# Optimization experiments

Hardware: AMD Instinct MI355X
Metric: run time of the kernel (lower is better)

The kernel has to match this reference:

```python
import jax, jax.numpy as jnp
import numpy as np

N_NODES = 100000
NEG_SLOPE = 0.2
EPS = 1e-16


def gat_conv(x, src, dst, W, a_src, a_dst, bias, heads, out_dim, concat):
    # x: [N, F]; src/dst: [Etot] (self loops already appended)
    N = x.shape[0]
    h = (x @ W).reshape(N, heads, out_dim)          # [N, H, D]
    alpha_src = jnp.einsum('nhd,hd->nh', h, a_src)  # [N, H]
    alpha_dst = jnp.einsum('nhd,hd->nh', h, a_dst)  # [N, H]
    e = alpha_src[src] + alpha_dst[dst]             # [E, H]
    e = jnp.where(e > 0, e, NEG_SLOPE * e)          # leaky_relu
    # segment softmax over incoming edges of each dst node
    m = jax.ops.segment_max(e, dst, num_segments=N)
    e = jnp.exp(e - m[dst])
    s = jax.ops.segment_sum(e, dst, num_segments=N)
    alpha = e / (s[dst] + EPS)                      # [E, H]
    msg = h[src] * alpha[:, :, None]                # [E, H, D]
    out = jax.ops.segment_sum(msg, dst, num_segments=N)  # [N, H, D]
    if concat:
        out = out.reshape(N, heads * out_dim)
    else:
        out = out.mean(axis=1)
    return out + bias


def setup_inputs() -> dict:
    key = jax.random.key(0)
    ks = jax.random.split(key, 10)
    F_in, H1, D1 = 256, 8, 8
    D2 = 256 // 2  # hidden_features // 2
    x = jax.random.normal(ks[0], (N_NODES, F_in), dtype=jnp.float32)
    edge_index = jax.random.randint(ks[1], (2, 1600000), 0, N_NODES, dtype=jnp.int64)
    sc1 = 1.0 / np.sqrt(F_in)
    sc2 = 1.0 / np.sqrt(H1 * D1)
    return {
        'x': x,
        'edge_index': edge_index,
        'W1': jax.random.normal(ks[2], (F_in, H1 * D1), dtype=jnp.float32) * sc1,
        'a_src1': jax.random.normal(ks[3], (H1, D1), dtype=jnp.float32) * 0.1,
        'a_dst1': jax.random.normal(ks[4], (H1, D1), dtype=jnp.float32) * 0.1,
        'b1': jnp.zeros((H1 * D1,), dtype=jnp.float32),
        'W2': jax.random.normal(ks[5], (H1 * D1, D2), dtype=jnp.float32) * sc2,
        'a_src2': jax.random.normal(ks[6], (1, D2), dtype=jnp.float32) * 0.1,
        'a_dst2': jax.random.normal(ks[7], (1, D2), dtype=jnp.float32) * 0.1,
        'b2': jnp.zeros((D2,), dtype=jnp.float32),
    }


def reference(x, edge_index, W1, a_src1, a_dst1, b1, W2, a_src2, a_dst2, b2):
    # GAT.encode in eval mode (dropout p=0.6 disabled)
    N = x.shape[0]
    loop = jnp.arange(N, dtype=edge_index.dtype)
    src = jnp.concatenate([edge_index[0], loop])  # PyG add_self_loops
    dst = jnp.concatenate([edge_index[1], loop])
    h = gat_conv(x, src, dst, W1, a_src1, a_dst1, b1, heads=8, out_dim=8, concat=True)
    h = jax.nn.elu(h)
    z = gat_conv(h, src, dst, W2, a_src2, a_dst2, b2, heads=1, out_dim=128, concat=False)
    return z
```

## Files before the change

kernel.cpp:

```cpp
#include <hip/hip_runtime.h>
#include <hip/hip_bf16.h>
#include <cstdint>

#define H1 8
#define C1 64
#define D2 128
#define FIN 256
#define NEG 0.2f
#define EPSS 1e-16f
#define CH 1024
#define XPAD 264
#define XQ 72
#define HP 68
#define NPBIN 128
#define TILEB 4096
#define MAXD1 128
#define MAXD2 256

template<typename T> __device__ __forceinline__ float toF(T v);
template<> __device__ __forceinline__ float toF<float>(float v) { return v; }
template<> __device__ __forceinline__ float toF<__hip_bfloat16>(__hip_bfloat16 v) { return __bfloat162float(v); }
template<typename T> __device__ __forceinline__ T fromF(float v);
template<> __device__ __forceinline__ float fromF<float>(float v) { return v; }
template<> __device__ __forceinline__ __hip_bfloat16 fromF<__hip_bfloat16>(float v) { return __float2bfloat16(v); }

__device__ __forceinline__ float bcast_lane(float v, int lane) {
    return __int_as_float(__builtin_amdgcn_readlane(__float_as_int(v), lane));
}

__device__ __forceinline__ unsigned pk_bf16(float lo, float hi) {
    unsigned a = (unsigned)__bfloat16_as_ushort(__float2bfloat16(lo));
    unsigned b = (unsigned)__bfloat16_as_ushort(__float2bfloat16(hi));
    return a | (b << 16);
}

__device__ __forceinline__ float bf16u_toF(unsigned short u) {
    unsigned v = ((unsigned)u) << 16;
    return __uint_as_float(v);
}

typedef __attribute__((ext_vector_type(8))) short bf16x8;
typedef __attribute__((ext_vector_type(4))) float f32x4;

__device__ __forceinline__ void chain_upd(float ev, float hv,
                                          float& m, float& s, float& a)
{
    float mn = fmaxf(m, ev);
    float sc = __expf(m - mn);
    float p  = __expf(ev - mn);
    s = fmaf(s, sc, p);
    a = fmaf(a, sc, p * hv);
    m = mn;
}

__global__ __launch_bounds__(256) void k_wcvt(const float* __restrict__ W1,
    unsigned short* __restrict__ Wb)
{
    int t = blockIdx.x * 256 + threadIdx.x;
    int c = t >> 7, kp = t & 127;
    if (c < C1) {
        float f0 = W1[(2 * kp) * C1 + c];
        float f1 = W1[(2 * kp + 1) * C1 + c];
        *reinterpret_cast<unsigned*>(&Wb[c * XPAD + 2 * kp]) = pk_bf16(f0, f1);
    }
}

__global__ __launch_bounds__(256) void k_w2cvt(const float* __restrict__ W2,
    unsigned short* __restrict__ W2b)
{
    int t = blockIdx.x * 256 + threadIdx.x;
    if (t < C1 * D2 / 2) {
        float f0 = W2[2 * t], f1 = W2[2 * t + 1];
        *reinterpret_cast<unsigned*>(&W2b[2 * t]) = pk_bf16(f0, f1);
    }
}

template<typename T>
__global__ __launch_bounds__(256) void k_gemm1(const float* __restrict__ x,
    const unsigned short* __restrict__ Wb, const float* __restrict__ a_src1,
    const float* __restrict__ a_dst1, T* __restrict__ h1,
    float* __restrict__ asrc1, float* __restrict__ adst1, int N)
{
    __shared__ alignas(16) char smem[2 * 64 * XQ * 2];
    unsigned short* Xs = (unsigned short*)smem;
    unsigned short* Wt = (unsigned short*)(smem + 64 * XQ * 2);
    int tid = threadIdx.x;
    int wave = tid >> 6, lane = tid & 63;
    int nodeBase = blockIdx.x * 64;
    int m = lane & 15, kg = lane >> 4;
    int arow = wave * 16 + m;

    f32x4 acc[4];
    #pragma unroll
    for (int t = 0; t < 4; ++t) acc[t] = (f32x4){0.f, 0.f, 0.f, 0.f};

    #pragma unroll
    for (int kh = 0; kh < 4; ++kh) {
        for (int i = tid; i < 512; i += 256) {
            int c = i >> 3, ch = i & 7;
            *reinterpret_cast<uint4*>(&Wt[c * XQ + ch * 8]) =
                *reinterpret_cast<const uint4*>(&Wb[c * XPAD + kh * 64 + ch * 8]);
        }
        for (int i = tid; i < 1024; i += 256) {
            int r = i >> 4, q = i & 15;
            int n = nodeBase + r;
            float4 v = (n < N) ? reinterpret_cast<const float4*>(x)[(size_t)n * 64 + kh * 16 + q]
                               : make_float4(0.f, 0.f, 0.f, 0.f);
            *reinterpret_cast<uint2*>(&Xs[r * XQ + q * 4]) =
                make_uint2(pk_bf16(v.x, v.y), pk_bf16(v.z, v.w));
        }
        __syncthreads();
        #pragma unroll
        for (int ks = 0; ks < 2; ++ks) {
            int k0 = ks * 32 + kg * 8;
            bf16x8 a = *reinterpret_cast<const bf16x8*>(&Xs[arow * XQ + k0]);
            #pragma unroll
            for (int t = 0; t < 4; ++t) {
                bf16x8 b = *reinterpret_cast<const bf16x8*>(&Wt[(t * 16 + m) * XQ + k0]);
                acc[t] = __builtin_amdgcn_mfma_f32_16x16x32_bf16(a, b, acc[t], 0, 0, 0);
            }
        }
        __syncthreads();
    }

    float* Hs = reinterpret_cast<float*>(smem);
    int crow = (lane >> 4) * 4;
    #pragma unroll
    for (int t = 0; t < 4; ++t)
        #pragma unroll
        for (int r = 0; r < 4; ++r)
            Hs[(wave * 16 + crow + r) * HP + t * 16 + m] = acc[t][r];
    __syncthreads();

    float as_l = a_src1[lane], ad_l = a_dst1[lane];
    int n0 = nodeBase + wave * 16;
    #pragma unroll
    for (int i = 0; i < 16; ++i) {
        int n = n0 + i;
        if (n >= N) break;
        float hv = Hs[(wave * 16 + i) * HP + lane];
        h1[(size_t)n * C1 + lane] = fromF<T>(hv);
        float vs = hv * as_l, vd = hv * ad_l;
        #pragma unroll
        for (int off = 1; off < 8; off <<= 1) {
            vs += __shfl_xor(vs, off);
            vd += __shfl_xor(vd, off);
        }
        if ((lane & 7) == 0) {
            asrc1[n * H1 + (lane >> 3)] = vs;
            adst1[n * H1 + (lane >> 3)] = vd;
        }
    }
}

__global__ __launch_bounds__(128) void k_wvec(const float* __restrict__ W2,
    const float* __restrict__ a_src2, const float* __restrict__ a_dst2,
    float* __restrict__ wsrc, float* __restrict__ wdst)
{
    int t = threadIdx.x;
    int k = t & 63;
    const float* a = (t < 64) ? a_src2 : a_dst2;
    float s = 0.f;
    for (int c = 0; c < D2; ++c) s = fmaf(W2[k * D2 + c], a[c], s);
    if (t < 64) wsrc[k] = s; else wdst[k] = s;
}

__global__ __launch_bounds__(256) void k_binhist(const int* __restrict__ ei, int E, int N,
    int nbins, int* __restrict__ binCnt)
{
    __shared__ int lcnt[1024];
    int tot = E + N;
    int t0 = blockIdx.x * TILEB;
    int cnt = min(TILEB, tot - t0);
    for (int i = threadIdx.x; i < nbins; i += 256) lcnt[i] = 0;
    __syncthreads();
    for (int i = threadIdx.x; i < cnt; i += 256) {
        int e = t0 + i;
        int dst = (e < E) ? ei[(size_t)E + e] : (e - E);
        atomicAdd(&lcnt[dst >> 7], 1);
    }
    __syncthreads();
    for (int i = threadIdx.x; i < nbins; i += 256)
        if (lcnt[i]) atomicAdd(&binCnt[i], lcnt[i]);
}

__global__ __launch_bounds__(256) void k_binscan(const int* __restrict__ binCnt,
    int* __restrict__ binOff, int* __restrict__ binCur, int nbins)
{
    __shared__ int wtot[4];
    int t = threadIdx.x, lane = t & 63, wave = t >> 6;
    int v[4];
    #pragma unroll
    for (int j = 0; j < 4; ++j) {
        int idx = t * 4 + j;
        v[j] = (idx < nbins) ? binCnt[idx] : 0;
    }
    int s = v[0] + v[1] + v[2] + v[3];
    int incl = s;
    #pragma unroll
    for (int off = 1; off < 64; off <<= 1) {
        int tt = __shfl_up(incl, off);
        if (lane >= off) incl += tt;
    }
    if (lane == 63) wtot[wave] = incl;
    __syncthreads();
    int woff = 0;
    #pragma unroll
    for (int w = 0; w < 4; ++w) if (w < wave) woff += wtot[w];
    int run = woff + incl - s;
    #pragma unroll
    for (int j = 0; j < 4; ++j) {
        int idx = t * 4 + j;
        if (idx < nbins) { binOff[idx] = run; binCur[idx] = run; }
        run += v[j];
    }
    if (t == 255) binOff[nbins] = woff + incl;
}

__global__ __launch_bounds__(256) void k_bin(const int* __restrict__ ei, int E, int N,
    int nbins, int* __restrict__ binCur, int* __restrict__ binned)
{
    __shared__ int recs[TILEB];
    __shared__ unsigned short bns[TILEB];
    __shared__ int lcnt[1024];
    __shared__ int lbase[1024];
    int tot = E + N;
    int t0 = blockIdx.x * TILEB;
    int cnt = min(TILEB, tot - t0);
    for (int i = threadIdx.x; i < nbins; i += 256) lcnt[i] = 0;
    __syncthreads();
    for (int i = threadIdx.x; i < cnt; i += 256) {
        int e = t0 + i;
        int src, dst;
        if (e < E) { src = ei[e]; dst = ei[(size_t)E + e]; }
        else       { src = e - E; dst = src; }
        int b = dst >> 7;
        recs[i] = src | ((dst & 127) << 17);
        bns[i] = (unsigned short)b;
        atomicAdd(&lcnt[b], 1);
    }
    __syncthreads();
    for (int i = threadIdx.x; i < nbins; i += 256) {
        int c = lcnt[i];
        if (c) lbase[i] = atomicAdd(&binCur[i], c);
        lcnt[i] = 0;
    }
    __syncthreads();
    for (int i = threadIdx.x; i < cnt; i += 256) {
        int b = bns[i];
        int lp = atomicAdd(&lcnt[b], 1);
        binned[lbase[b] + lp] = recs[i];
    }
}

__global__ __launch_bounds__(256) void k_binptr(const int* __restrict__ binOff,
    const int* __restrict__ binned, int* __restrict__ ptr,
    int* __restrict__ edge_src, int N, int nbins)
{
    __shared__ int cnt[NPBIN];
    __shared__ int cur[NPBIN];
    __shared__ int w0tot;
    int b = blockIdx.x, t = threadIdx.x;
    int s0 = binOff[b], s1 = binOff[b + 1];
    if (t < NPBIN) cnt[t] = 0;
    __syncthreads();
    for (int i = s0 + t; i < s1; i += 256)
        atomicAdd(&cnt[binned[i] >> 17], 1);
    __syncthreads();
    int v = 0, incl = 0;
    if (t < NPBIN) {
        int lane = t & 63;
        v = cnt[t];
        incl = v;
        #pragma unroll
        for (int off = 1; off < 64; off <<= 1) {
            int tt = __shfl_up(incl, off);
            if (lane >= off) incl += tt;
        }
        if (t == 63) w0tot = incl;
    }
    __syncthreads();
    if (t < NPBIN) {
        int base = s0 + ((t >= 64) ? w0tot : 0);
        int excl = base + incl - v;
        int node = b * NPBIN + t;
        if (node < N) ptr[node] = excl;
        cur[t] = excl;
    }
    if (b == nbins - 1 && t == 0) ptr[N] = s1;
    __syncthreads();
    for (int i = s0 + t; i < s1; i += 256) {
        int rec = binned[i];
        int p = atomicAdd(&cur[rec >> 17], 1);
        edge_src[p] = rec & 0x1FFFF;
    }
}

__global__ void k_count(const int* __restrict__ ei, int E, int N,
                        int* __restrict__ deg)
{
    int tot = E + N;
    for (int e = blockIdx.x * blockDim.x + threadIdx.x; e < tot;
         e += gridDim.x * blockDim.x) {
        int dst = (e < E) ? ei[(size_t)E + e] : (e - E);
        atomicAdd(&deg[dst], 1);
    }
}

__global__ void k_scatter(const int* __restrict__ ei, int E, int N,
                          int* __restrict__ cursor, int* __restrict__ edge_src)
{
    int tot = E + N;
    for (int e = blockIdx.x * blockDim.x + threadIdx.x; e < tot;
         e += gridDim.x * blockDim.x) {
        int src, dst;
        if (e < E) { src = ei[e]; dst = ei[(size_t)E + e]; }
        else       { src = e - E; dst = e - E; }
        int pos = atomicAdd(&cursor[dst], 1);
        edge_src[pos] = src;
    }
}

__global__ __launch_bounds__(256) void k_scanA(const int* __restrict__ deg,
    int* __restrict__ ptr, int* __restrict__ chunkSum)
{
    __shared__ int wtot[4];
    int b = blockIdx.x, t = threadIdx.x;
    int lane = t & 63, wave = t >> 6;
    int4 v = reinterpret_cast<const int4*>(deg + (size_t)b * CH)[t];
    int s = v.x + v.y + v.z + v.w;
    int incl = s;
    #pragma unroll
    for (int off = 1; off < 64; off <<= 1) {
        int tt = __shfl_up(incl, off);
        if (lane >= off) incl += tt;
    }
    if (lane == 63) wtot[wave] = incl;
    __syncthreads();
    int woff = 0;
    #pragma unroll
    for (int w = 0; w < 4; ++w) if (w < wave) woff += wtot[w];
    int excl = woff + incl - s;
    int i0 = b * CH + t * 4;
    ptr[i0 + 0] = excl;
    ptr[i0 + 1] = excl + v.x;
    ptr[i0 + 2] = excl + v.x + v.y;
    ptr[i0 + 3] = excl + v.x + v.y + v.z;
    if (t == 255) chunkSum[b] = woff + incl;
}

__global__ void k_scanB(const int* __restrict__ chunkSum, int* __restrict__ chunkOff,
                        int NB, int* __restrict__ ptrN)
{
    if (threadIdx.x == 0) {
        int c = 0;
        for (int b = 0; b < NB; ++b) { chunkOff[b] = c; c += chunkSum[b]; }
        *ptrN = c;
    }
}

__global__ __launch_bounds__(256) void k_scanC(int* __restrict__ ptr,
    int* __restrict__ cursor, const int* __restrict__ chunkOff, int N)
{
    int b = blockIdx.x;
    int off = chunkOff[b];
    int i0 = b * CH + threadIdx.x * 4;
    #pragma unroll
    for (int k = 0; k < 4; ++k) {
        int i = i0 + k;
        if (i < N) { int v = ptr[i] + off; ptr[i] = v; cursor[i] = v; }
    }
}

template<typename T>
__global__ __launch_bounds__(256) void k_agg1(const int* __restrict__ ptr,
    const int* __restrict__ edge_src, const T* __restrict__ h1,
    const float* __restrict__ asrc1, const float* __restrict__ adst1,
    const float* __restrict__ b1, const float* __restrict__ wsrc,
    const float* __restrict__ wdst, T* __restrict__ hmid,
    float* __restrict__ asrc2, float* __restrict__ adst2, int N)
{
    __shared__ float S1[4 * MAXD1 * H1];
    int wave = threadIdx.x >> 6, lane = threadIdx.x & 63;
    float* st = S1 + wave * (MAXD1 * H1);
    int n = blockIdx.x * 4 + wave;
    if (n >= N) return;
    int start = ptr[n], end = ptr[n + 1];
    int deg = end - start;
    int h = lane >> 3;
    float o;

    if (deg <= MAXD1) {
        int e_loc = lane >> 3, hh = lane & 7;
        float adsth = adst1[n * H1 + hh];
        float mloc = -1e30f;
        for (int eb = start, base = 0; eb < end; eb += 8, base += 64) {
            int e = eb + e_loc;
            float ev = -1e30f;
            if (e < end) {
                int s = edge_src[e];
                ev = asrc1[s * H1 + hh] + adsth;
                ev = ev > 0.f ? ev : NEG * ev;
                st[base + lane] = ev;
            }
            mloc = fmaxf(mloc, ev);
        }
        mloc = fmaxf(mloc, __shfl_xor(mloc, 8));
        mloc = fmaxf(mloc, __shfl_xor(mloc, 16));
        mloc = fmaxf(mloc, __shfl_xor(mloc, 32));
        __builtin_amdgcn_wave_barrier();
        float sloc = 0.f;
        for (int eb = start, base = 0; eb < end; eb += 8, base += 64) {
            if (eb + e_loc < end) {
                float p = __expf(st[base + lane] - mloc);
                st[base + lane] = p;
                sloc += p;
            }
        }
        sloc += __shfl_xor(sloc, 8);
        sloc += __shfl_xor(sloc, 16);
        sloc += __shfl_xor(sloc, 32);
        float inv = 1.f / (sloc + EPSS);
        __builtin_amdgcn_wave_barrier();
        float inv_c = __shfl(inv, h);

        float a0 = 0.f, a1 = 0.f, a2 = 0.f, a3 = 0.f;
        float a4 = 0.f, a5 = 0.f, a6 = 0.f, a7 = 0.f;
        int e = start;
        for (; e + 8 <= end; e += 8) {
            int r = e - start;
            int i0 = edge_src[e + 0]; int i1 = edge_src[e + 1];
            int i2 = edge_src[e + 2]; int i3 = edge_src[e + 3];
            int i4 = edge_src[e + 4]; int i5 = edge_src[e + 5];
            int i6 = edge_src[e + 6]; int i7 = edge_src[e + 7];
            float w0 = st[(r + 0) * H1 + h]; float w1 = st[(r + 1) * H1 + h];
            float w2 = st[(r + 2) * H1 + h]; float w3 = st[(r + 3) * H1 + h];
            float w4 = st[(r + 4) * H1 + h]; float w5 = st[(r + 5) * H1 + h];
            float w6 = st[(r + 6) * H1 + h]; float w7 = st[(r + 7) * H1 + h];
            a0 = fmaf(w0, toF(h1[((size_t)(unsigned)i0 << 6) + lane]), a0);
            a1 = fmaf(w1, toF(h1[((size_t)(unsigned)i1 << 6) + lane]), a1);
            a2 = fmaf(w2, toF(h1[((size_t)(unsigned)i2 << 6) + lane]), a2);
            a3 = fmaf(w3, toF(h1[((size_t)(unsigned)i3 << 6) + lane]), a3);
            a4 = fmaf(w4, toF(h1[((size_t)(unsigned)i4 << 6) + lane]), a4);
            a5 = fmaf(w5, toF(h1[((size_t)(unsigned)i5 << 6) + lane]), a5);
            a6 = fmaf(w6, toF(h1[((size_t)(unsigned)i6 << 6) + lane]), a6);
            a7 = fmaf(w7, toF(h1[((size_t)(unsigned)i7 << 6) + lane]), a7);
        }
        for (; e < end; ++e) {
            int s = edge_src[e];
            a0 = fmaf(st[(e - start) * H1 + h],
                      toF(h1[((size_t)(unsigned)s << 6) + lane]), a0);
        }
        float acc = ((a0 + a1) + (a2 + a3)) + ((a4 + a5) + (a6 + a7));
        o = acc * inv_c;
    } else {
        float adst = adst1[n * H1 + h];
        float m[8], ss[8], aa[8];
        #pragma unroll
        for (int j = 0; j < 8; ++j) { m[j] = -1e30f; ss[j] = 0.f; aa[j] = 0.f; }
        int e = start;
        for (; e + 8 <= end; e += 8) {
            int idx[8];
            #pragma unroll
            for (int j = 0; j < 8; ++j) idx[j] = edge_src[e + j];
            #pragma unroll
            for (int j = 0; j < 8; ++j) {
                float t = asrc1[idx[j] * H1 + h] + adst;
                t = t > 0.f ? t : NEG * t;
                chain_upd(t, toF(h1[((size_t)(unsigned)idx[j] << 6) + lane]),
                          m[j], ss[j], aa[j]);
            }
        }
        for (; e < end; ++e) {
            int s = edge_src[e];
            float t = asrc1[s * H1 + h] + adst;
            t = t > 0.f ? t : NEG * t;
            chain_upd(t, toF(h1[((size_t)(unsigned)s << 6) + lane]), m[0], ss[0], aa[0]);
        }
        float M = fmaxf(fmaxf(fmaxf(m[0], m[1]), fmaxf(m[2], m[3])),
                        fmaxf(fmaxf(m[4], m[5]), fmaxf(m[6], m[7])));
        float sum = 0.f, acc = 0.f;
        #pragma unroll
        for (int j = 0; j < 8; ++j) {
            float sc = __expf(m[j] - M);
            sum = fmaf(ss[j], sc, sum);
            acc = fmaf(aa[j], sc, acc);
        }
        o = acc / (sum + EPSS);
    }

    o = o + b1[lane];
    o = o > 0.f ? o : (expf(o) - 1.f);
    hmid[(size_t)n * C1 + lane] = fromF<T>(o);
    float vs = o * wsrc[lane];
    float vd = o * wdst[lane];
    #pragma unroll
    for (int off = 1; off < 64; off <<= 1) {
        vs += __shfl_xor(vs, off);
        vd += __shfl_xor(vd, off);
    }
    if (lane == 0) { asrc2[n] = vs; adst2[n] = vd; }
}

template<typename T>
__global__ __launch_bounds__(256) void k_agg2out(const int* __restrict__ ptr,
    const int* __restrict__ edge_src, const T* __restrict__ hmid,
    const float* __restrict__ asrc2, const float* __restrict__ adst2,
    const unsigned short* __restrict__ W2b, const float* __restrict__ b2,
    float* __restrict__ out, int N)
{
    __shared__ unsigned short Ws[C1 * D2];
    __shared__ float S2[4 * MAXD2];
    for (int i = threadIdx.x; i < C1 * D2 / 8; i += 256)
        reinterpret_cast<uint4*>(Ws)[i] = reinterpret_cast<const uint4*>(W2b)[i];
    __syncthreads();

    int wave = threadIdx.x >> 6, lane = threadIdx.x & 63;
    float* st = S2 + wave * MAXD2;
    int n = blockIdx.x * 4 + wave;
    if (n >= N) return;
    int start = ptr[n], end = ptr[n + 1];
    int deg = end - start;
    float adst = adst2[n];
    float aggv;

    if (deg <= MAXD2) {
        float mloc = -1e30f;
        for (int e = start + lane; e < end; e += 64) {
            int s = edge_src[e];
            float ev = asrc2[s] + adst;
            ev = ev > 0.f ? ev : NEG * ev;
            st[e - start] = ev;
            mloc = fmaxf(mloc, ev);
        }
        #pragma unroll
        for (int off = 1; off < 64; off <<= 1)
            mloc = fmaxf(mloc, __shfl_xor(mloc, off));
        __builtin_amdgcn_wave_barrier();
        float sloc = 0.f;
        for (int e = start + lane; e < end; e += 64) {
            float p = __expf(st[e - start] - mloc);
            st[e - start] = p;
            sloc += p;
        }
        #pragma unroll
        for (int off = 1; off < 64; off <<= 1)
            sloc += __shfl_xor(sloc, off);
        float inv = 1.f / (sloc + EPSS);
        __builtin_amdgcn_wave_barrier();

        float a0 = 0.f, a1 = 0.f, a2 = 0.f, a3 = 0.f;
        float a4 = 0.f, a5 = 0.f, a6 = 0.f, a7 = 0.f;
        int e = start;
        for (; e + 8 <= end; e += 8) {
            int r = e - start;
            int i0 = edge_src[e + 0]; int i1 = edge_src[e + 1];
            int i2 = edge_src[e + 2]; int i3 = edge_src[e + 3];
            int i4 = edge_src[e + 4]; int i5 = edge_src[e + 5];
            int i6 = edge_src[e + 6]; int i7 = edge_src[e + 7];
            a0 = fmaf(st[r + 0], toF(hmid[((size_t)(unsigned)i0 << 6) + lane]), a0);
            a1 = fmaf(st[r + 1], toF(hmid[((size_t)(unsigned)i1 << 6) + lane]), a1);
            a2 = fmaf(st[r + 2], toF(hmid[((size_t)(unsigned)i2 << 6) + lane]), a2);
            a3 = fmaf(st[r + 3], toF(hmid[((size_t)(unsigned)i3 << 6) + lane]), a3);
            a4 = fmaf(st[r + 4], toF(hmid[((size_t)(unsigned)i4 << 6) + lane]), a4);
            a5 = fmaf(st[r + 5], toF(hmid[((size_t)(unsigned)i5 << 6) + lane]), a5);
            a6 = fmaf(st[r + 6], toF(hmid[((size_t)(unsigned)i6 << 6) + lane]), a6);
            a7 = fmaf(st[r + 7], toF(hmid[((size_t)(unsigned)i7 << 6) + lane]), a7);
        }
        for (; e < end; ++e) {
            int s = edge_src[e];
            a0 = fmaf(st[e - start], toF(hmid[((size_t)(unsigned)s << 6) + lane]), a0);
        }
        float acc = ((a0 + a1) + (a2 + a3)) + ((a4 + a5) + (a6 + a7));
        aggv = acc * inv;
    } else {
        float m[8], ss[8], aa[8];
        #pragma unroll
        for (int j = 0; j < 8; ++j) { m[j] = -1e30f; ss[j] = 0.f; aa[j] = 0.f; }
        int e = start;
        for (; e + 8 <= end; e += 8) {
            int idx[8];
            #pragma unroll
            for (int j = 0; j < 8; ++j) idx[j] = edge_src[e + j];
            #pragma unroll
            for (int j = 0; j < 8; ++j) {
                float t = asrc2[idx[j]] + adst;
                t = t > 0.f ? t : NEG * t;
                chain_upd(t, toF(hmid[((size_t)(unsigned)idx[j] << 6) + lane]),
                          m[j], ss[j], aa[j]);
            }
        }
        for (; e < end; ++e) {
            int s = edge_src[e];
            float t = asrc2[s] + adst;
            t = t > 0.f ? t : NEG * t;
            chain_upd(t, toF(hmid[((size_t)(unsigned)s << 6) + lane]), m[0], ss[0], aa[0]);
        }
        float M = fmaxf(fmaxf(fmaxf(m[0], m[1]), fmaxf(m[2], m[3])),
                        fmaxf(fmaxf(m[4], m[5]), fmaxf(m[6], m[7])));
        float sum = 0.f, acc = 0.f;
        #pragma unroll
        for (int j = 0; j < 8; ++j) {
            float sc = __expf(m[j] - M);
            sum = fmaf(ss[j], sc, sum);
            acc = fmaf(aa[j], sc, acc);
        }
        aggv = acc / (sum + EPSS);
    }

    float acc0 = 0.f, acc1 = 0.f;
    #pragma unroll
    for (int k = 0; k < 64; ++k) {
        float xk = bcast_lane(aggv, k);
        float w0 = bf16u_toF(Ws[k * D2 + lane]);
        float w1 = bf16u_toF(Ws[k * D2 + 64 + lane]);
        acc0 = fmaf(xk, w0, acc0);
        acc1 = fmaf(xk, w1, acc1);
    }
    out[(size_t)n * D2 + lane]      = acc0 + b2[lane];
    out[(size_t)n * D2 + 64 + lane] = acc1 + b2[64 + lane];
}

extern "C" void kernel_launch(void* const* d_in, const int* in_sizes, int n_in,
                              void* d_out, int out_size, void* d_ws, size_t ws_size,
                              hipStream_t stream)
{
    const float* x      = (const float*)d_in[0];
    const int*   ei     = (const int*)d_in[1];
    const float* W1     = (const float*)d_in[2];
    const float* a_src1 = (const float*)d_in[3];
    const float* a_dst1 = (const float*)d_in[4];
    const float* b1     = (const float*)d_in[5];
    const float* W2     = (const float*)d_in[6];
    const float* a_src2 = (const float*)d_in[7];
    const float* a_dst2 = (const float*)d_in[8];
    const float* b2     = (const float*)d_in[9];
    float* out = (float*)d_out;

    const int N = in_sizes[0] / FIN;
    const int E = in_sizes[1] / 2;
    const int Etot = E + N;
    const int NB = (N + CH - 1) / CH;
    const size_t NP = (size_t)NB * CH;

    const size_t common =
        ((size_t)N * H1 * 4 + 255 & ~(size_t)255) * 2 +
        (((size_t)N * 4 + 255) & ~(size_t)255) * 2 +
        512 +
        (((size_t)NP * 4 + 255) & ~(size_t)255) * 2 +
        (((size_t)(NP + 1) * 4 + 255) & ~(size_t)255) +
        (((size_t)NB * 4 + 255) & ~(size_t)255) * 2 +
        (((size_t)Etot * 4 + 255) & ~(size_t)255) +
        (64 * XPAD * 2 + 256) +
        (C1 * D2 * 2 + 256) +
        4096;
    const bool f32path = ws_size >= common + 2 * ((size_t)N * C1 * 4 + 256);

    char* ws = (char*)d_ws;
    size_t off = 0;
    auto alloc = [&](size_t bytes) -> void* {
        void* p = ws + off;
        off = (off + bytes + 255) & ~(size_t)255;
        return p;
    };
    const size_t es = f32path ? 4 : 2;
    void*  h1v    = alloc((size_t)N * C1 * es);
    void*  hmidv  = alloc((size_t)N * C1 * es);
    float* asrc1  = (float*)alloc((size_t)N * H1 * 4);
    float* adst1  = (float*)alloc((size_t)N * H1 * 4);
    float* asrc2  = (float*)alloc((size_t)N * 4);
    float* adst2  = (float*)alloc((size_t)N * 4);
    float* wsrc   = (float*)alloc(64 * 4);
    float* wdst   = (float*)alloc(64 * 4);
    int*   deg    = (int*)alloc(NP * 4);
    int*   ptr    = (int*)alloc((NP + 1) * 4);
    int*   cursor = (int*)alloc(NP * 4);
    int*   chunkSum = (int*)alloc((size_t)NB * 4);
    int*   chunkOff = (int*)alloc((size_t)NB * 4);
    int*   edge_src = (int*)alloc((size_t)Etot * 4);
    unsigned short* Wb  = (unsigned short*)alloc(64 * XPAD * 2);
    unsigned short* W2b = (unsigned short*)alloc(C1 * D2 * 2);

    const int nodeBlocks = (N + 3) / 4;
    const int g1Blocks = (N + 63) / 64;

    k_wcvt<<<32, 256, 0, stream>>>(W1, Wb);
    k_w2cvt<<<16, 256, 0, stream>>>(W2, W2b);

    const int nbins = (N + NPBIN - 1) / NPBIN;
    const bool binpath = (N <= (1 << 17)) &&
                         ((size_t)Etot * 4 <= (size_t)N * C1 * es);
    if (binpath) {
        int* binned = (int*)h1v;
        int* binCnt = (int*)hmidv;
        int* binOff = binCnt + 1056;
        int* binCur = binOff + 1056;
        const int binBlocks = (Etot + TILEB - 1) / TILEB;
        hipMemsetAsync(binCnt, 0, (size_t)nbins * 4, stream);
        k_binhist<<<binBlocks, 256, 0, stream>>>(ei, E, N, nbins, binCnt);
        k_binscan<<<1, 256, 0, stream>>>(binCnt, binOff, binCur, nbins);
        k_bin<<<binBlocks, 256, 0, stream>>>(ei, E, N, nbins, binCur, binned);
        k_binptr<<<nbins, 256, 0, stream>>>(binOff, binned, ptr, edge_src, N, nbins);
    } else {
        hipMemsetAsync(deg, 0, NP * 4, stream);
        k_count<<<2048, 256, 0, stream>>>(ei, E, N, deg);
        k_scanA<<<NB, 256, 0, stream>>>(deg, ptr, chunkSum);
        k_scanB<<<1, 64, 0, stream>>>(chunkSum, chunkOff, NB, ptr + N);
        k_scanC<<<NB, 256, 0, stream>>>(ptr, cursor, chunkOff, N);
        k_scatter<<<2048, 256, 0, stream>>>(ei, E, N, cursor, edge_src);
    }

    k_wvec<<<1, 128, 0, stream>>>(W2, a_src2, a_dst2, wsrc, wdst);

    if (f32path) {
        float* h1 = (float*)h1v; float* hmid = (float*)hmidv;
        k_gemm1<float><<<g1Blocks, 256, 0, stream>>>(x, Wb, a_src1, a_dst1, h1, asrc1, adst1, N);
        k_agg1<float><<<nodeBlocks, 256, 0, stream>>>(ptr, edge_src, h1, asrc1, adst1, b1,
                                                      wsrc, wdst, hmid, asrc2, adst2, N);
        k_agg2out<float><<<nodeBlocks, 256, 0, stream>>>(ptr, edge_src, hmid, asrc2, adst2,
                                                         W2b, b2, out, N);
    } else {
        __hip_bfloat16* h1 = (__hip_bfloat16*)h1v; __hip_bfloat16* hmid = (__hip_bfloat16*)hmidv;
        k_gemm1<__hip_bfloat16><<<g1Blocks, 256, 0, stream>>>(x, Wb, a_src1, a_dst1, h1, asrc1, adst1, N);
        k_agg1<__hip_bfloat16><<<nodeBlocks, 256, 0, stream>>>(ptr, edge_src, h1, asrc1, adst1, b1,
                                                               wsrc, wdst, hmid, asrc2, adst2, N);
        k_agg2out<__hip_bfloat16><<<nodeBlocks, 256, 0, stream>>>(ptr, edge_src, hmid, asrc2, adst2,
                                                                  W2b, b2, out, N);
    }
}
```

Before: 335.6 us.

## Split layer-2 aggregation from output GEMM and merge weight prep kernels

Splits the fused aggregation-plus-projection kernel into two. The aggregation kernel writes the 64-wide aggregated vector to a scratch buffer, and a separate GEMM kernel computes 8 nodes per wave, so each shared-memory W2 load is reused across several nodes. The aggregation kernel no longer loads 16 KB of weights into LDS per block of 4 nodes. The three small weight-prep kernels become one launch. In exchange, the aggregated intermediate makes an extra round trip through global memory and one more kernel launch is added.

```diff
diff --git a/kernel.cpp b/kernel.cpp
--- a/kernel.cpp
+++ b/kernel.cpp
@@ -9,6 +9,8 @@
 #define NEG 0.2f
 #define EPSS 1e-16f
 #define CH 1024
+#define NPW2 8
+#define NPB2 32
 #define XPAD 264
 #define XQ 72
 #define HP 68
@@ -53,25 +55,36 @@
     m = mn;
 }
 
-__global__ __launch_bounds__(256) void k_wcvt(const float* __restrict__ W1,
-    unsigned short* __restrict__ Wb)
-{
-    int t = blockIdx.x * 256 + threadIdx.x;
-    int c = t >> 7, kp = t & 127;
-    if (c < C1) {
-        float f0 = W1[(2 * kp) * C1 + c];
-        float f1 = W1[(2 * kp + 1) * C1 + c];
-        *reinterpret_cast<unsigned*>(&Wb[c * XPAD + 2 * kp]) = pk_bf16(f0, f1);
-    }
-}
-
-__global__ __launch_bounds__(256) void k_w2cvt(const float* __restrict__ W2,
-    unsigned short* __restrict__ W2b)
-{
-    int t = blockIdx.x * 256 + threadIdx.x;
-    if (t < C1 * D2 / 2) {
-        float f0 = W2[2 * t], f1 = W2[2 * t + 1];
-        *reinterpret_cast<unsigned*>(&W2b[2 * t]) = pk_bf16(f0, f1);
+__global__ __launch_bounds__(256) void k_wprep(const float* __restrict__ W1,
+    const float* __restrict__ W2, const float* __restrict__ a_src2,
+    const float* __restrict__ a_dst2, unsigned short* __restrict__ Wb,
+    unsigned short* __restrict__ W2b, float* __restrict__ wsrc,
+    float* __restrict__ wdst)
+{
+    int b = blockIdx.x;
+    if (b < 32) {
+        int t = b * 256 + threadIdx.x;
+        int c = t >> 7, kp = t & 127;
+        if (c < C1) {
+            float f0 = W1[(2 * kp) * C1 + c];
+            float f1 = W1[(2 * kp + 1) * C1 + c];
+            *reinterpret_cast<unsigned*>(&Wb[c * XPAD + 2 * kp]) = pk_bf16(f0, f1);
+        }
+    } else if (b < 48) {
+        int t = (b - 32) * 256 + threadIdx.x;
+        if (t < C1 * D2 / 2) {
+            float f0 = W2[2 * t], f1 = W2[2 * t + 1];
+            *reinterpret_cast<unsigned*>(&W2b[2 * t]) = pk_bf16(f0, f1);
+        }
+    } else {
+        int t = threadIdx.x;
+        if (t < 128) {
+            int k = t & 63;
+            const float* a = (t < 64) ? a_src2 : a_dst2;
+            float s = 0.f;
+            for (int c = 0; c < D2; ++c) s = fmaf(W2[k * D2 + c], a[c], s);
+            if (t < 64) wsrc[k] = s; else wdst[k] = s;
+        }
     }
 }
 
@@ -151,18 +164,6 @@
             adst1[n * H1 + (lane >> 3)] = vd;
         }
     }
-}
-
-__global__ __launch_bounds__(128) void k_wvec(const float* __restrict__ W2,
-    const float* __restrict__ a_src2, const float* __restrict__ a_dst2,
-    float* __restrict__ wsrc, float* __restrict__ wdst)
-{
-    int t = threadIdx.x;
-    int k = t & 63;
-    const float* a = (t < 64) ? a_src2 : a_dst2;
-    float s = 0.f;
-    for (int c = 0; c < D2; ++c) s = fmaf(W2[k * D2 + c], a[c], s);
-    if (t < 64) wsrc[k] = s; else wdst[k] = s;
 }
 
 __global__ __launch_bounds__(256) void k_binhist(const int* __restrict__ ei, int E, int N,
@@ -503,18 +504,12 @@
 }
 
 template<typename T>
-__global__ __launch_bounds__(256) void k_agg2out(const int* __restrict__ ptr,
+__global__ __launch_bounds__(256) void k_agg2(const int* __restrict__ ptr,
     const int* __restrict__ edge_src, const T* __restrict__ hmid,
     const float* __restrict__ asrc2, const float* __restrict__ adst2,
-    const unsigned short* __restrict__ W2b, const float* __restrict__ b2,
-    float* __restrict__ out, int N)
-{
-    __shared__ unsigned short Ws[C1 * D2];
+    T* __restrict__ aggv_out, int N)
+{
     __shared__ float S2[4 * MAXD2];
-    for (int i = threadIdx.x; i < C1 * D2 / 8; i += 256)
-        reinterpret_cast<uint4*>(Ws)[i] = reinterpret_cast<const uint4*>(W2b)[i];
-    __syncthreads();
-
     int wave = threadIdx.x >> 6, lane = threadIdx.x & 63;
     float* st = S2 + wave * MAXD2;
     int n = blockIdx.x * 4 + wave;
@@ -607,18 +602,53 @@
         }
         aggv = acc / (sum + EPSS);
     }
-
-    float acc0 = 0.f, acc1 = 0.f;
-    #pragma unroll
+    aggv_out[(size_t)n * C1 + lane] = fromF<T>(aggv);
+}
+
+template<typename T>
+__global__ __launch_bounds__(256) void k_gemm2(const T* __restrict__ aggv,
+    const unsigned short* __restrict__ W2b, const float* __restrict__ b2,
+    float* __restrict__ out, int N)
+{
+    __shared__ unsigned short Ws[C1 * D2];
+    for (int i = threadIdx.x; i < C1 * D2 / 8; i += 256)
+        reinterpret_cast<uint4*>(Ws)[i] = reinterpret_cast<const uint4*>(W2b)[i];
+
+    int wave = threadIdx.x >> 6, lane = threadIdx.x & 63;
+    int n0 = blockIdx.x * NPB2 + wave * NPW2;
+
+    float av[NPW2];
+    #pragma unroll
+    for (int j = 0; j < NPW2; ++j) {
+        int n = n0 + j;
+        av[j] = (n < N) ? toF(aggv[(size_t)n * C1 + lane]) : 0.f;
+    }
+    __syncthreads();
+
+    float acc0[NPW2], acc1[NPW2];
+    #pragma unroll
+    for (int j = 0; j < NPW2; ++j) { acc0[j] = 0.f; acc1[j] = 0.f; }
+
+    #pragma unroll 4
     for (int k = 0; k < 64; ++k) {
-        float xk = bcast_lane(aggv, k);
         float w0 = bf16u_toF(Ws[k * D2 + lane]);
         float w1 = bf16u_toF(Ws[k * D2 + 64 + lane]);
-        acc0 = fmaf(xk, w0, acc0);
-        acc1 = fmaf(xk, w1, acc1);
-    }
-    out[(size_t)n * D2 + lane]      = acc0 + b2[lane];
-    out[(size_t)n * D2 + 64 + lane] = acc1 + b2[64 + lane];
+        #pragma unroll
+        for (int j = 0; j < NPW2; ++j) {
+            float xk = bcast_lane(av[j], k);
+            acc0[j] = fmaf(xk, w0, acc0[j]);
+            acc1[j] = fmaf(xk, w1, acc1[j]);
+        }
+    }
+
+    float bb0 = b2[lane], bb1 = b2[64 + lane];
+    #pragma unroll
+    for (int j = 0; j < NPW2; ++j) {
+        int n = n0 + j;
+        if (n >= N) continue;
+        out[(size_t)n * D2 + lane]      = acc0[j] + bb0;
+        out[(size_t)n * D2 + 64 + lane] = acc1[j] + bb1;
+    }
 }
 
 extern "C" void kernel_launch(void* const* d_in, const int* in_sizes, int n_in,
@@ -683,9 +713,9 @@
 
     const int nodeBlocks = (N + 3) / 4;
     const int g1Blocks = (N + 63) / 64;
-
-    k_wcvt<<<32, 256, 0, stream>>>(W1, Wb);
-    k_w2cvt<<<16, 256, 0, stream>>>(W2, W2b);
+    const int g2Blocks = (N + NPB2 - 1) / NPB2;
+
+    k_wprep<<<49, 256, 0, stream>>>(W1, W2, a_src2, a_dst2, Wb, W2b, wsrc, wdst);
 
     const int nbins = (N + NPBIN - 1) / NPBIN;
     const bool binpath = (N <= (1 << 17)) &&
@@ -710,21 +740,21 @@
         k_scatter<<<2048, 256, 0, stream>>>(ei, E, N, cursor, edge_src);
     }
 
-    k_wvec<<<1, 128, 0, stream>>>(W2, a_src2, a_dst2, wsrc, wdst);
-
     if (f32path) {
         float* h1 = (float*)h1v; float* hmid = (float*)hmidv;
         k_gemm1<float><<<g1Blocks, 256, 0, stream>>>(x, Wb, a_src1, a_dst1, h1, asrc1, adst1, N);
         k_agg1<float><<<nodeBlocks, 256, 0, stream>>>(ptr, edge_src, h1, asrc1, adst1, b1,
                                                       wsrc, wdst, hmid, asrc2, adst2, N);
-        k_agg2out<float><<<nodeBlocks, 256, 0, stream>>>(ptr, edge_src, hmid, asrc2, adst2,
-                                                         W2b, b2, out, N);
+        float* aggv = (float*)h1v;
+        k_agg2<float><<<nodeBlocks, 256, 0, stream>>>(ptr, edge_src, hmid, asrc2, adst2, aggv, N);
+        k_gemm2<float><<<g2Blocks, 256, 0, stream>>>(aggv, W2b, b2, out, N);
     } else {
         __hip_bfloat16* h1 = (__hip_bfloat16*)h1v; __hip_bfloat16* hmid = (__hip_bfloat16*)hmidv;
         k_gemm1<__hip_bfloat16><<<g1Blocks, 256, 0, stream>>>(x, Wb, a_src1, a_dst1, h1, asrc1, adst1, N);
         k_agg1<__hip_bfloat16><<<nodeBlocks, 256, 0, stream>>>(ptr, edge_src, h1, asrc1, adst1, b1,
                                                                wsrc, wdst, hmid, asrc2, adst2, N);
-        k_agg2out<__hip_bfloat16><<<nodeBlocks, 256, 0, stream>>>(ptr, edge_src, hmid, asrc2, adst2,
-                                                                  W2b, b2, out, N);
-    }
-}
+        __hip_bfloat16* aggv = (__hip_bfloat16*)h1v;
+        k_agg2<__hip_bfloat16><<<nodeBlocks, 256, 0, stream>>>(ptr, edge_src, hmid, asrc2, adst2, aggv, N);
+        k_gemm2<__hip_bfloat16><<<g2Blocks, 256, 0, stream>>>(aggv, W2b, b2, out, N);
+    }
+}
```

Result: no change. 336.2 us (+0.2%).
